# Performance work log

Hardware: AMD Instinct MI355X
Metric: run time of the kernel (lower is better)

The kernel has to match this reference:

```python
import jax, jax.numpy as jnp
import numpy as np

N = 1_000_000
C = 100


def setup_inputs() -> dict:
    key = jax.random.key(0)
    k1, k2 = jax.random.split(key)
    score = jax.random.normal(k1, (N,), dtype=jnp.float32)
    label = jax.random.randint(k2, (N,), 0, C, dtype=jnp.int64)
    return {"score": score, "label": label, "class_num": C, "epsilon_num": 95}


def reference(score, label, class_num, epsilon_num):
    # Faithful translation of Logit_Linear.get_th (epsilon = epsilon_num/100).
    epsilon = epsilon_num / 100.0
    n = score.shape[0]
    class_id = jnp.arange(class_num)
    # s_n_classes: per-class counts (scatter_add of ones over labels)
    s_n_classes = jax.ops.segment_sum(
        jnp.ones((n,), dtype=score.dtype), label, num_segments=class_num
    )
    max_ele = jnp.max(score)
    # mat[i, c] = (label[i] == c); fill non-class entries with the global max
    mat = label[:, None] == class_id[None, :]          # [N, C] bool
    score_mat = jnp.where(mat, score[:, None], max_ele)  # [N, C]
    score_mat = jnp.sort(score_mat, axis=0)              # msort: sort along N
    idx = (s_n_classes * (1.0 - epsilon)).astype(jnp.int32)  # quantile row per class
    th = score_mat[idx, class_id]                        # [C]
    return th
```

## Files before the change

### kernel.cpp

```cpp
#include <hip/hip_runtime.h>


#define MAXC      128
#define NB        256
#define T1        1024
#define SLICE_CAP 4096
#define STAGE_CAP 12288
#define SORT_CAP  (1u << 21)

__device__ unsigned int g_skey[SORT_CAP];
__device__ unsigned int g_pd[MAXC * NB * 64];
__device__ unsigned int g_csrc[MAXC * NB];
__device__ unsigned int g_blockmax[NB];

__device__ __forceinline__ unsigned int fkey(float f) {
    unsigned int u = __float_as_uint(f);
    return (u & 0x80000000u) ? ~u : (u | 0x80000000u);
}
__device__ __forceinline__ float ikey(unsigned int u) {
    unsigned int b = (u & 0x80000000u) ? (u ^ 0x80000000u) : ~u;
    return __uint_as_float(b);
}

__device__ __forceinline__ void scan256_wave0(const unsigned int* h,
                                              unsigned int* s, int t) {
    if (t < 64) {
        unsigned int a0 = h[4 * t], a1 = h[4 * t + 1];
        unsigned int a2 = h[4 * t + 2], a3 = h[4 * t + 3];
        unsigned int loc = a0 + a1 + a2 + a3;
        unsigned int run = loc;
#pragma unroll
        for (int off = 1; off < 64; off <<= 1) {
            unsigned int v = (unsigned int)__shfl_up((int)run, off, 64);
            if (t >= off) run += v;
        }
        unsigned int excl = run - loc;
        s[4 * t]     = excl + a0;
        s[4 * t + 1] = excl + a0 + a1;
        s[4 * t + 2] = excl + a0 + a1 + a2;
        s[4 * t + 3] = excl + loc;
    }
}

__global__ __launch_bounds__(T1) void sort_kernel(const float* __restrict__ score,
                                                  const int* __restrict__ label,
                                                  int n, const int* __restrict__ cnp) {
    __shared__ unsigned int  raw[SLICE_CAP];
    __shared__ unsigned int  skey[SLICE_CAP];
    __shared__ unsigned char lab[SLICE_CAP];
    __shared__ unsigned int  table[MAXC * 128];
    __shared__ unsigned int  wsum[T1 / 64];
    __shared__ unsigned int  wmax[T1 / 64];
    const int t = threadIdx.x;
    const int b = blockIdx.x;
    const int lane = t & 63, wid = t >> 6;
    int cn = *cnp; if (cn > MAXC) cn = MAXC;

    for (int i = t; i < MAXC * 128; i += T1) table[i] = 0u;
    __syncthreads();

    const int per = ((n + NB - 1) / NB + 3) & ~3;
    const int i0 = b * per;
    const int i1 = min(n, i0 + per);
    const int len = (i1 > i0) ? (i1 - i0) : 0;
    const int nv = len >> 2;
    const float4* s4 = (const float4*)(score + i0);
    const int4*   l4 = (const int4*)(label + i0);
    unsigned int lmax = 0u;

    for (int j = t; j < nv; j += T1) {
        float4 s = s4[j]; int4 l = l4[j];
        float sv[4] = {s.x, s.y, s.z, s.w};
        int   lv[4] = {l.x, l.y, l.z, l.w};
#pragma unroll
        for (int q = 0; q < 4; ++q) {
            unsigned int u = fkey(sv[q]);
            int c = lv[q] & (MAXC - 1);
            int idx = 4 * j + q;
            raw[idx] = u;
            lab[idx] = (unsigned char)c;
            lmax = lmax > u ? lmax : u;
            atomicAdd(&table[(c << 7) | (u >> 25)], ((u >> 24) & 1u) ? 65536u : 1u);
        }
    }
    for (int i = (nv << 2) + t; i < len; i += T1) {
        unsigned int u = fkey(score[i0 + i]);
        int c = label[i0 + i] & (MAXC - 1);
        raw[i] = u;
        lab[i] = (unsigned char)c;
        lmax = lmax > u ? lmax : u;
        atomicAdd(&table[(c << 7) | (u >> 25)], ((u >> 24) & 1u) ? 65536u : 1u);
    }
#pragma unroll
    for (int off = 32; off; off >>= 1) {
        unsigned int o = (unsigned int)__shfl_xor((int)lmax, off, 64);
        lmax = lmax > o ? lmax : o;
    }
    if (lane == 0) wmax[wid] = lmax;
    __syncthreads();

    for (int idx = t; idx < (cn << 6); idx += T1) {
        int c = idx >> 6, q = idx & 63;
        unsigned int w0 = table[(c << 7) | (2 * q)];
        unsigned int w1 = table[(c << 7) | (2 * q + 1)];
        g_pd[((size_t)c * NB + b) * 64 + q] =
            (w0 & 0xFFu) | (((w0 >> 16) & 0xFFu) << 8) |
            ((w1 & 0xFFu) << 16) | (((w1 >> 16) & 0xFFu) << 24);
    }

    constexpr int W = (MAXC * 128) / T1;
    unsigned int lsum = 0u;
#pragma unroll
    for (int w2 = 0; w2 < W; ++w2) {
        unsigned int v = table[t * W + w2];
        lsum += (v & 0xFFFFu) + (v >> 16);
    }
    unsigned int run = lsum;
#pragma unroll
    for (int off = 1; off < 64; off <<= 1) {
        unsigned int v = (unsigned int)__shfl_up((int)run, off, 64);
        if (lane >= off) run += v;
    }
    if (lane == 63) wsum[wid] = run;
    __syncthreads();
    if (t < T1 / 64) {
        unsigned int v = wsum[t], r2 = v;
#pragma unroll
        for (int off = 1; off < T1 / 64; off <<= 1) {
            unsigned int x = (unsigned int)__shfl_up((int)r2, off, 64);
            if (t >= off) r2 += x;
        }
        wsum[t] = r2 - v;
    }
    __syncthreads();
    unsigned int running = wsum[wid] + (run - lsum);
#pragma unroll
    for (int w2 = 0; w2 < W; ++w2) {
        unsigned int v = table[t * W + w2];
        unsigned int lo = v & 0xFFFFu, hi = v >> 16;
        table[t * W + w2] = running | ((running + lo) << 16);
        running += lo + hi;
    }
    __syncthreads();

    if (t < cn) g_csrc[t * NB + b] = (unsigned int)i0 + (table[t << 7] & 0xFFFFu);

    for (int j = t; j < len; j += T1) {
        unsigned int u = raw[j];
        int c = lab[j];
        unsigned int d = u >> 24;
        unsigned int old = atomicAdd(&table[(c << 7) | (d >> 1)],
                                     (d & 1u) ? 65536u : 1u);
        unsigned int pos = (d & 1u) ? (old >> 16) : (old & 0xFFFFu);
        skey[pos] = u;
    }
    __syncthreads();

    for (int j = t; j < len; j += T1) g_skey[i0 + j] = skey[j];
    if (t == 0) {
        unsigned int m = wmax[0];
        for (int w3 = 1; w3 < T1 / 64; ++w3) m = m > wmax[w3] ? m : wmax[w3];
        g_blockmax[b] = m;
    }
}

__global__ __launch_bounds__(T1) void select_kernel(const int* __restrict__ cnp,
                                                    const int* __restrict__ epsp,
                                                    float* __restrict__ out) {
    int cn = *cnp; if (cn > MAXC) cn = MAXC;
    const int c = blockIdx.x;
    if (c >= cn) return;
    const int t = threadIdx.x;
    __shared__ unsigned int red[16 * 256];
    __shared__ unsigned int hist[256];
    __shared__ unsigned int scn[256];
    __shared__ unsigned int lenb[NB];
    __shared__ unsigned int offb[NB];
    __shared__ unsigned int baseb[NB];
    __shared__ unsigned int csrc[NB];
    __shared__ unsigned int sel2[2];
    __shared__ unsigned int stage[STAGE_CAP];

    {
        const int q = t & 63, chunk = t >> 6;
        unsigned int s0 = 0u, s1 = 0u, s2 = 0u, s3 = 0u;
        const unsigned int* p = g_pd + ((size_t)c * NB + chunk * 16) * 64 + q;
        for (int j = 0; j < 16; ++j) {
            unsigned int w = p[j * 64];
            s0 += w & 0xFFu;         s1 += (w >> 8) & 0xFFu;
            s2 += (w >> 16) & 0xFFu; s3 += w >> 24;
        }
        red[chunk * 256 + 4 * q + 0] = s0;
        red[chunk * 256 + 4 * q + 1] = s1;
        red[chunk * 256 + 4 * q + 2] = s2;
        red[chunk * 256 + 4 * q + 3] = s3;
    }
    __syncthreads();
    if (t < 256) {
        unsigned int s = 0u;
#pragma unroll
        for (int ch = 0; ch < 16; ++ch) s += red[ch * 256 + t];
        hist[t] = s;
    }
    __syncthreads();
    scan256_wave0(hist, scn, t);
    __syncthreads();
    const unsigned int m = scn[255];

    double eps = (double)(*epsp) / 100.0;
    float fac = (float)(1.0 - eps);
    int k = (int)((float)m * fac);

    if (m == 0u || k >= (int)m) {
        if (t < 256) hist[t] = g_blockmax[t];
        __syncthreads();
        for (int off = 128; off; off >>= 1) {
            if (t < off) { unsigned int a = hist[t + off]; if (a > hist[t]) hist[t] = a; }
            __syncthreads();
        }
        if (t == 0) out[c] = ikey(hist[0]);
        return;
    }

    if (t < 256) {
        unsigned int incl = scn[t], excl = incl - hist[t];
        if ((unsigned)k >= excl && (unsigned)k < incl) { sel2[0] = (unsigned)t; sel2[1] = excl; }
    }
    __syncthreads();
    const unsigned int d0 = sel2[0];
    int rem = k - (int)sel2[1];
    __syncthreads();

    if (t < NB) {
        const unsigned int* p = g_pd + ((size_t)c * NB + t) * 64;
        unsigned int off = 0u;
        const unsigned int nq = d0 >> 2;
        for (unsigned int j = 0; j < nq; ++j) {
            unsigned int w = p[j];
            off += (w & 0xFFu) + ((w >> 8) & 0xFFu) + ((w >> 16) & 0xFFu) + (w >> 24);
        }
        unsigned int w2 = p[nq];
        unsigned int r = d0 & 3u;
        if (r > 0u) off += w2 & 0xFFu;
        if (r > 1u) off += (w2 >> 8) & 0xFFu;
        if (r > 2u) off += (w2 >> 16) & 0xFFu;
        lenb[t] = (w2 >> (8u * r)) & 0xFFu;
        offb[t] = off;
        csrc[t] = g_csrc[c * NB + t];
    }
    __syncthreads();
    scan256_wave0(lenb, scn, t);
    __syncthreads();
    if (t < NB) baseb[t] = scn[t] - lenb[t];
    __syncthreads();
    const unsigned int m2 = scn[NB - 1];
    const int staged = (m2 <= STAGE_CAP);

    if (staged) {
        const int b = t >> 2, q = t & 3;
        const unsigned int L = lenb[b], s0 = csrc[b] + offb[b], dd = baseb[b];
        for (unsigned int j = q; j < L; j += 4) stage[dd + j] = g_skey[s0 + j];
        __syncthreads();
    }

    unsigned int pref = d0 << 24;
    for (int shift = 16; shift >= 0; shift -= 8) {
        if (t < 256) hist[t] = 0u;
        __syncthreads();
        if (staged) {
            for (unsigned int j = t; j < m2; j += T1) {
                unsigned int u = stage[j];
                if ((u >> (shift + 8)) == (pref >> (shift + 8)))
                    atomicAdd(&hist[(u >> shift) & 255u], 1u);
            }
        } else {
            const int b = t >> 2, q = t & 3;
            const unsigned int L = lenb[b], s0 = csrc[b] + offb[b];
            for (unsigned int j = q; j < L; j += 4) {
                unsigned int u = g_skey[s0 + j];
                if ((u >> (shift + 8)) == (pref >> (shift + 8)))
                    atomicAdd(&hist[(u >> shift) & 255u], 1u);
            }
        }
        __syncthreads();
        scan256_wave0(hist, scn, t);
        __syncthreads();
        if (t < 256) {
            unsigned int incl = scn[t], excl = incl - hist[t];
            if ((unsigned)rem >= excl && (unsigned)rem < incl) { sel2[0] = (unsigned)t; sel2[1] = excl; }
        }
        __syncthreads();
        rem -= (int)sel2[1];
        pref |= sel2[0] << shift;
        __syncthreads();
    }
    if (t == 0) out[c] = ikey(pref);
}

extern "C" void kernel_launch(void* const* d_in, const int* in_sizes, int n_in,
                              void* d_out, int out_size, void* d_ws, size_t ws_size,
                              hipStream_t stream) {
    const float* score = (const float*)d_in[0];
    const int*   label = (const int*)d_in[1];
    const int*   cnp   = (const int*)d_in[2];
    const int*   epsp  = (const int*)d_in[3];
    float*       out   = (float*)d_out;
    int n = in_sizes[0];
    int gsel = out_size > 0 ? out_size : MAXC;
    if (gsel > MAXC) gsel = MAXC;

    sort_kernel  <<<NB,   T1, 0, stream>>>(score, label, n, cnp);
    select_kernel<<<gsel, T1, 0, stream>>>(cnp, epsp, out);
}
```

Baseline: 28.76 us.

## Bucket keys by class only and use a 64-bin first radix digit

The sort kernel now groups keys only by class with per-class atomic cursors instead of by class and top digit. This removes the 16K-entry table scan and keeps the per-block histogram at 64 digits. The select kernel reads each class's full segment via new per-block lengths rather than only the selected-digit sub-bucket. As a result the later radix passes scan every element of the class, and an extra 2-bit pass is needed to finish the 32-bit key. The intent is to cut shared-memory, prefix-scan and g_pd traffic in exchange for more refinement work in the select kernel.

```diff
diff --git a/kernel.cpp b/kernel.cpp
--- a/kernel.cpp
+++ b/kernel.cpp
@@ -7,10 +7,14 @@
 #define SLICE_CAP 4096
 #define STAGE_CAP 12288
 #define SORT_CAP  (1u << 21)
+#define NDIG      64
+#define QPC       (NDIG / 4)
+#define WPC       (NDIG / 2)
 
 __device__ unsigned int g_skey[SORT_CAP];
-__device__ unsigned int g_pd[MAXC * NB * 64];
+__device__ unsigned int g_pd[MAXC * NB * QPC];
 __device__ unsigned int g_csrc[MAXC * NB];
+__device__ unsigned int g_clen[MAXC * NB];
 __device__ unsigned int g_blockmax[NB];
 
 __device__ __forceinline__ unsigned int fkey(float f) {
@@ -48,15 +52,17 @@
     __shared__ unsigned int  raw[SLICE_CAP];
     __shared__ unsigned int  skey[SLICE_CAP];
     __shared__ unsigned char lab[SLICE_CAP];
-    __shared__ unsigned int  table[MAXC * 128];
-    __shared__ unsigned int  wsum[T1 / 64];
+    __shared__ unsigned int  table[MAXC * WPC];
+    __shared__ unsigned int  cnt[MAXC];
+    __shared__ unsigned int  exc[MAXC];
+    __shared__ unsigned int  cur[MAXC];
     __shared__ unsigned int  wmax[T1 / 64];
     const int t = threadIdx.x;
     const int b = blockIdx.x;
     const int lane = t & 63, wid = t >> 6;
     int cn = *cnp; if (cn > MAXC) cn = MAXC;
 
-    for (int i = t; i < MAXC * 128; i += T1) table[i] = 0u;
+    for (int i = t; i < MAXC * WPC; i += T1) table[i] = 0u;
     __syncthreads();
 
     const int per = ((n + NB - 1) / NB + 3) & ~3;
@@ -80,7 +86,8 @@
             raw[idx] = u;
             lab[idx] = (unsigned char)c;
             lmax = lmax > u ? lmax : u;
-            atomicAdd(&table[(c << 7) | (u >> 25)], ((u >> 24) & 1u) ? 65536u : 1u);
+            unsigned int d = u >> 26;
+            atomicAdd(&table[(c << 5) | (d >> 1)], (d & 1u) ? 65536u : 1u);
         }
     }
     for (int i = (nv << 2) + t; i < len; i += T1) {
@@ -89,7 +96,8 @@
         raw[i] = u;
         lab[i] = (unsigned char)c;
         lmax = lmax > u ? lmax : u;
-        atomicAdd(&table[(c << 7) | (u >> 25)], ((u >> 24) & 1u) ? 65536u : 1u);
+        unsigned int d = u >> 26;
+        atomicAdd(&table[(c << 5) | (d >> 1)], (d & 1u) ? 65536u : 1u);
     }
 #pragma unroll
     for (int off = 32; off; off >>= 1) {
@@ -99,64 +107,50 @@
     if (lane == 0) wmax[wid] = lmax;
     __syncthreads();
 
-    for (int idx = t; idx < (cn << 6); idx += T1) {
-        int c = idx >> 6, q = idx & 63;
-        unsigned int w0 = table[(c << 7) | (2 * q)];
-        unsigned int w1 = table[(c << 7) | (2 * q + 1)];
-        g_pd[((size_t)c * NB + b) * 64 + q] =
+    for (int idx = t; idx < cn * QPC; idx += T1) {
+        int c = idx >> 4, q = idx & 15;
+        unsigned int w0 = table[(c << 5) | (2 * q)];
+        unsigned int w1 = table[(c << 5) | (2 * q + 1)];
+        g_pd[((size_t)c * NB + b) * QPC + q] =
             (w0 & 0xFFu) | (((w0 >> 16) & 0xFFu) << 8) |
             ((w1 & 0xFFu) << 16) | (((w1 >> 16) & 0xFFu) << 24);
     }
-
-    constexpr int W = (MAXC * 128) / T1;
-    unsigned int lsum = 0u;
-#pragma unroll
-    for (int w2 = 0; w2 < W; ++w2) {
-        unsigned int v = table[t * W + w2];
-        lsum += (v & 0xFFFFu) + (v >> 16);
-    }
-    unsigned int run = lsum;
-#pragma unroll
-    for (int off = 1; off < 64; off <<= 1) {
-        unsigned int v = (unsigned int)__shfl_up((int)run, off, 64);
-        if (lane >= off) run += v;
-    }
-    if (lane == 63) wsum[wid] = run;
-    __syncthreads();
-    if (t < T1 / 64) {
-        unsigned int v = wsum[t], r2 = v;
-#pragma unroll
-        for (int off = 1; off < T1 / 64; off <<= 1) {
-            unsigned int x = (unsigned int)__shfl_up((int)r2, off, 64);
-            if (t >= off) r2 += x;
-        }
-        wsum[t] = r2 - v;
-    }
-    __syncthreads();
-    unsigned int running = wsum[wid] + (run - lsum);
-#pragma unroll
-    for (int w2 = 0; w2 < W; ++w2) {
-        unsigned int v = table[t * W + w2];
-        unsigned int lo = v & 0xFFFFu, hi = v >> 16;
-        table[t * W + w2] = running | ((running + lo) << 16);
-        running += lo + hi;
-    }
-    __syncthreads();
-
-    if (t < cn) g_csrc[t * NB + b] = (unsigned int)i0 + (table[t << 7] & 0xFFFFu);
+    if (t < MAXC) {
+        unsigned int s = 0u;
+        for (int j = 0; j < WPC; ++j) {
+            unsigned int w = table[(t << 5) | ((j + t) & 31)];
+            s += (w & 0xFFFFu) + (w >> 16);
+        }
+        cnt[t] = s;
+    }
+    __syncthreads();
+
+    if (t < 64) {
+        unsigned int a0 = cnt[2 * t], a1 = cnt[2 * t + 1];
+        unsigned int loc = a0 + a1, run = loc;
+#pragma unroll
+        for (int off = 1; off < 64; off <<= 1) {
+            unsigned int v = (unsigned int)__shfl_up((int)run, off, 64);
+            if (t >= off) run += v;
+        }
+        unsigned int excl = run - loc;
+        exc[2 * t] = excl;      exc[2 * t + 1] = excl + a0;
+        cur[2 * t] = excl;      cur[2 * t + 1] = excl + a0;
+    }
+    __syncthreads();
 
     for (int j = t; j < len; j += T1) {
-        unsigned int u = raw[j];
         int c = lab[j];
-        unsigned int d = u >> 24;
-        unsigned int old = atomicAdd(&table[(c << 7) | (d >> 1)],
-                                     (d & 1u) ? 65536u : 1u);
-        unsigned int pos = (d & 1u) ? (old >> 16) : (old & 0xFFFFu);
-        skey[pos] = u;
+        unsigned int p = atomicAdd(&cur[c], 1u);
+        skey[p] = raw[j];
     }
     __syncthreads();
 
     for (int j = t; j < len; j += T1) g_skey[i0 + j] = skey[j];
+    if (t < cn) {
+        g_csrc[t * NB + b] = (unsigned int)i0 + exc[t];
+        g_clen[t * NB + b] = cnt[t];
+    }
     if (t == 0) {
         unsigned int m = wmax[0];
         for (int w3 = 1; w3 < T1 / 64; ++w3) m = m > wmax[w3] ? m : wmax[w3];
@@ -171,41 +165,47 @@
     const int c = blockIdx.x;
     if (c >= cn) return;
     const int t = threadIdx.x;
-    __shared__ unsigned int red[16 * 256];
+    __shared__ unsigned int red[64 * 65];
     __shared__ unsigned int hist[256];
     __shared__ unsigned int scn[256];
     __shared__ unsigned int lenb[NB];
-    __shared__ unsigned int offb[NB];
-    __shared__ unsigned int baseb[NB];
-    __shared__ unsigned int csrc[NB];
+    __shared__ unsigned int csrcS[NB];
+    __shared__ unsigned int rbase[NB];
     __shared__ unsigned int sel2[2];
     __shared__ unsigned int stage[STAGE_CAP];
 
     {
-        const int q = t & 63, chunk = t >> 6;
+        const int q = t & 15, chunk = t >> 4;
         unsigned int s0 = 0u, s1 = 0u, s2 = 0u, s3 = 0u;
-        const unsigned int* p = g_pd + ((size_t)c * NB + chunk * 16) * 64 + q;
-        for (int j = 0; j < 16; ++j) {
-            unsigned int w = p[j * 64];
+        const unsigned int* p = g_pd + ((size_t)c * NB + chunk * 4) * QPC + q;
+        for (int j = 0; j < 4; ++j) {
+            unsigned int w = p[j * QPC];
             s0 += w & 0xFFu;         s1 += (w >> 8) & 0xFFu;
             s2 += (w >> 16) & 0xFFu; s3 += w >> 24;
         }
-        red[chunk * 256 + 4 * q + 0] = s0;
-        red[chunk * 256 + 4 * q + 1] = s1;
-        red[chunk * 256 + 4 * q + 2] = s2;
-        red[chunk * 256 + 4 * q + 3] = s3;
-    }
-    __syncthreads();
-    if (t < 256) {
+        red[chunk * 65 + 4 * q + 0] = s0;
+        red[chunk * 65 + 4 * q + 1] = s1;
+        red[chunk * 65 + 4 * q + 2] = s2;
+        red[chunk * 65 + 4 * q + 3] = s3;
+    }
+    __syncthreads();
+    if (t < 64) {
         unsigned int s = 0u;
-#pragma unroll
-        for (int ch = 0; ch < 16; ++ch) s += red[ch * 256 + t];
+        for (int ch = 0; ch < 64; ++ch) s += red[ch * 65 + t];
         hist[t] = s;
     }
     __syncthreads();
-    scan256_wave0(hist, scn, t);
-    __syncthreads();
-    const unsigned int m = scn[255];
+    if (t < 64) {
+        unsigned int v = hist[t], run = v;
+#pragma unroll
+        for (int off = 1; off < 64; off <<= 1) {
+            unsigned int x = (unsigned int)__shfl_up((int)run, off, 64);
+            if (t >= off) run += x;
+        }
+        scn[t] = run;
+    }
+    __syncthreads();
+    const unsigned int m = scn[63];
 
     double eps = (double)(*epsp) / 100.0;
     float fac = (float)(1.0 - eps);
@@ -222,7 +222,7 @@
         return;
     }
 
-    if (t < 256) {
+    if (t < 64) {
         unsigned int incl = scn[t], excl = incl - hist[t];
         if ((unsigned)k >= excl && (unsigned)k < incl) { sel2[0] = (unsigned)t; sel2[1] = excl; }
     }
@@ -232,50 +232,35 @@
     __syncthreads();
 
     if (t < NB) {
-        const unsigned int* p = g_pd + ((size_t)c * NB + t) * 64;
-        unsigned int off = 0u;
-        const unsigned int nq = d0 >> 2;
-        for (unsigned int j = 0; j < nq; ++j) {
-            unsigned int w = p[j];
-            off += (w & 0xFFu) + ((w >> 8) & 0xFFu) + ((w >> 16) & 0xFFu) + (w >> 24);
-        }
-        unsigned int w2 = p[nq];
-        unsigned int r = d0 & 3u;
-        if (r > 0u) off += w2 & 0xFFu;
-        if (r > 1u) off += (w2 >> 8) & 0xFFu;
-        if (r > 2u) off += (w2 >> 16) & 0xFFu;
-        lenb[t] = (w2 >> (8u * r)) & 0xFFu;
-        offb[t] = off;
-        csrc[t] = g_csrc[c * NB + t];
+        lenb[t]  = g_clen[c * NB + t];
+        csrcS[t] = g_csrc[c * NB + t];
     }
     __syncthreads();
     scan256_wave0(lenb, scn, t);
     __syncthreads();
-    if (t < NB) baseb[t] = scn[t] - lenb[t];
-    __syncthreads();
-    const unsigned int m2 = scn[NB - 1];
-    const int staged = (m2 <= STAGE_CAP);
-
+    if (t < NB) rbase[t] = scn[t] - lenb[t];
+    __syncthreads();
+    const int staged = (m <= STAGE_CAP);
     if (staged) {
-        const int b = t >> 2, q = t & 3;
-        const unsigned int L = lenb[b], s0 = csrc[b] + offb[b], dd = baseb[b];
+        const int bb = t >> 2, q = t & 3;
+        const unsigned int L = lenb[bb], s0 = csrcS[bb], dd = rbase[bb];
         for (unsigned int j = q; j < L; j += 4) stage[dd + j] = g_skey[s0 + j];
         __syncthreads();
     }
 
-    unsigned int pref = d0 << 24;
-    for (int shift = 16; shift >= 0; shift -= 8) {
+    unsigned int pref = d0 << 26;
+    for (int shift = 18; shift >= 2; shift -= 8) {
         if (t < 256) hist[t] = 0u;
         __syncthreads();
         if (staged) {
-            for (unsigned int j = t; j < m2; j += T1) {
+            for (unsigned int j = t; j < m; j += T1) {
                 unsigned int u = stage[j];
                 if ((u >> (shift + 8)) == (pref >> (shift + 8)))
                     atomicAdd(&hist[(u >> shift) & 255u], 1u);
             }
         } else {
-            const int b = t >> 2, q = t & 3;
-            const unsigned int L = lenb[b], s0 = csrc[b] + offb[b];
+            const int bb = t >> 2, q = t & 3;
+            const unsigned int L = lenb[bb], s0 = csrcS[bb];
             for (unsigned int j = q; j < L; j += 4) {
                 unsigned int u = g_skey[s0 + j];
                 if ((u >> (shift + 8)) == (pref >> (shift + 8)))
@@ -294,7 +279,31 @@
         pref |= sel2[0] << shift;
         __syncthreads();
     }
-    if (t == 0) out[c] = ikey(pref);
+    if (t < 4) hist[t] = 0u;
+    __syncthreads();
+    if (staged) {
+        for (unsigned int j = t; j < m; j += T1) {
+            unsigned int u = stage[j];
+            if ((u >> 2) == (pref >> 2)) atomicAdd(&hist[u & 3u], 1u);
+        }
+    } else {
+        const int bb = t >> 2, q = t & 3;
+        const unsigned int L = lenb[bb], s0 = csrcS[bb];
+        for (unsigned int j = q; j < L; j += 4) {
+            unsigned int u = g_skey[s0 + j];
+            if ((u >> 2) == (pref >> 2)) atomicAdd(&hist[u & 3u], 1u);
+        }
+    }
+    __syncthreads();
+    if (t == 0) {
+        unsigned int cum = 0u, dsel = 3u;
+        for (unsigned int dd = 0; dd < 4; ++dd) {
+            unsigned int h = hist[dd];
+            if (cum + h > (unsigned)rem) { dsel = dd; break; }
+            cum += h;
+        }
+        out[c] = ikey(pref | dsel);
+    }
 }
 
 extern "C" void kernel_launch(void* const* d_in, const int* in_sizes, int n_in,
```

Measured after the change: 27.40 us. -4.7%, faster.
